# Kernel tuning notes

Hardware: AMD Instinct MI355X
Metric: run time of the kernel (lower is better)

## Reference

```python
import jax, jax.numpy as jnp
import numpy as np

CHANNELS = 256
TEMPERATURE = 0.1
VAR_LAMBDA = 0.001
N = 4096


def _pairwise_sq_dist(x, y):
    xx = jnp.sum(x * x, axis=-1)[:, None]
    yy = jnp.sum(y * y, axis=-1)[None, :]
    xy = jnp.einsum('ic,jc->ij', x, y)
    return xx + yy - 2.0 * xy


def _tcc_loss(emb_a, emb_b, idxes):
    scale = 1.0 / (CHANNELS * TEMPERATURE)
    sim_ab = -_pairwise_sq_dist(emb_a, emb_b) * scale            # [Na, Nb]
    softmaxed_sim_ab = jax.nn.softmax(sim_ab, axis=-1)
    soft_nn = softmaxed_sim_ab @ emb_b                            # [Na, C]
    sim_ba = -_pairwise_sq_dist(soft_nn, emb_a) * scale           # [Na, Na]
    beta = jax.nn.softmax(sim_ba, axis=-1)
    preds = jnp.sum(beta * idxes, axis=-1, keepdims=True)         # [Na, 1]
    pred_var = jnp.sum((idxes - preds) ** 2 * beta, axis=1)       # [Na]
    pred_var_log = jnp.log(pred_var)
    squared_error = (idxes - jnp.squeeze(preds, -1)) ** 2
    return jnp.sum(jnp.exp(-pred_var_log) * squared_error + VAR_LAMBDA * pred_var_log)


def setup_inputs() -> dict:
    key = jax.random.key(0)
    k1, k2 = jax.random.split(key)
    emb_a = jax.random.normal(k1, (1, N, CHANNELS), dtype=jnp.float32)
    emb_b = jax.random.normal(k2, (1, N, CHANNELS), dtype=jnp.float32)
    idx_a = jnp.arange(N, dtype=jnp.float32)
    idx_b = jnp.arange(N, dtype=jnp.float32)
    return {"emb_a": emb_a, "emb_b": emb_b, "idx_a": idx_a, "idx_b": idx_b}


def reference(emb_a, emb_b, idx_a, idx_b):
    a = jnp.squeeze(emb_a, 0)
    b = jnp.squeeze(emb_b, 0)
    loss_ab = _tcc_loss(a, b, idx_a)
    loss_ba = _tcc_loss(b, a, idx_b)
    return (loss_ab + loss_ba) / (a.shape[0] + b.shape[0])
```

## Files before the change

kernel.cpp:

```cpp
#include <hip/hip_runtime.h>

#define NTOT 4096
#define CH 256
#define SCALE 0.0390625f
#define LAM 0.001f

typedef unsigned short u16;
typedef __attribute__((ext_vector_type(8))) short short8;
typedef __attribute__((ext_vector_type(4))) float floatx4;

__device__ __forceinline__ float wave_sum64(float v) {
  #pragma unroll
  for (int o = 32; o; o >>= 1) v += __shfl_down(v, o, 64);
  return v;
}
__device__ __forceinline__ u16 f2bf(float f) {
  unsigned u = __float_as_uint(f);
  u += 0x7fffu + ((u >> 16) & 1u);
  return (u16)(u >> 16);
}
__device__ __forceinline__ float bf2f(u16 h) {
  return __uint_as_float(((unsigned)h) << 16);
}
__device__ __forceinline__ void gload_lds(const u16* g, void* l) {
  __builtin_amdgcn_global_load_lds((const __attribute__((address_space(1))) void*)g,
                                   (__attribute__((address_space(3))) void*)l, 16, 0, 0);
}
__device__ __forceinline__ void mm4x4(const short8 (&av)[4], const short8 (&bv)[4],
                                      floatx4 (&acc)[4][4]) {
  #pragma unroll
  for (int m = 0; m < 4; ++m)
    #pragma unroll
    for (int n = 0; n < 4; ++n)
      acc[m][n] = __builtin_amdgcn_mfma_f32_16x16x32_bf16(av[m], bv[n], acc[m][n], 0, 0, 0);
}

__global__ __launch_bounds__(64) void cvt_norm_k(const float* __restrict__ a,
                                                 const float* __restrict__ b,
                                                 u16* __restrict__ ab, u16* __restrict__ bb,
                                                 float* __restrict__ na, float* __restrict__ nb) {
  int row = blockIdx.x;
  const float* src; u16* dst; float* nd;
  if (row < NTOT) { src = a; dst = ab; nd = na; }
  else { row -= NTOT; src = b; dst = bb; nd = nb; }
  const float4 v = *reinterpret_cast<const float4*>(src + (size_t)row * CH + threadIdx.x * 4);
  const u16 h0 = f2bf(v.x), h1 = f2bf(v.y), h2 = f2bf(v.z), h3 = f2bf(v.w);
  uint2 st;
  st.x = (unsigned)h0 | ((unsigned)h1 << 16);
  st.y = (unsigned)h2 | ((unsigned)h3 << 16);
  *reinterpret_cast<uint2*>(dst + (size_t)row * CH + threadIdx.x * 4) = st;
  const float f0 = bf2f(h0), f1 = bf2f(h1), f2 = bf2f(h2), f3 = bf2f(h3);
  float s = f0 * f0 + f1 * f1 + f2 * f2 + f3 * f3;
  s = wave_sum64(s);
  if (threadIdx.x == 0) nd[row] = s;
}

__global__ __launch_bounds__(256) void transpose2_k(const u16* __restrict__ ab,
                                                    const u16* __restrict__ bb,
                                                    u16* __restrict__ at, u16* __restrict__ bt) {
  const u16* __restrict__ src = blockIdx.z ? bb : ab;
  u16* __restrict__ dst = blockIdx.z ? bt : at;
  __shared__ u16 t[32][33];
  const int bx = blockIdx.x * 32, by = blockIdx.y * 32;
  const int lx = threadIdx.x & 31, ly = threadIdx.x >> 5;
  #pragma unroll
  for (int i = 0; i < 32; i += 8)
    t[ly + i][lx] = src[(size_t)(by + ly + i) * CH + bx + lx];
  __syncthreads();
  #pragma unroll
  for (int i = 0; i < 32; i += 8)
    dst[(size_t)(bx + ly + i) * NTOT + by + lx] = t[lx][ly + i];
}

__global__ __launch_bounds__(256, 2) void gemm_exp_k(const u16* __restrict__ abf,
                                                     const u16* __restrict__ bbf,
                                                     const float* __restrict__ na,
                                                     const float* __restrict__ nb,
                                                     u16* __restrict__ E,
                                                     float* __restrict__ dnp) {
  const int wg = blockIdx.x;
  const int dir = wg >> 10;
  const int w = wg & 1023;
  const int xcd = w & 7;
  const int local = w >> 3;
  const int bx = local & 31;
  const int by = xcd * 4 + (local >> 5);

  const u16* __restrict__ A = dir ? bbf : abf;
  const u16* __restrict__ B = dir ? abf : bbf;
  const float* __restrict__ ny = dir ? na : nb;
  E += (size_t)dir * NTOT * NTOT;
  dnp += (size_t)dir * NTOT * 64;

  __shared__ u16 As[2][128][64];
  __shared__ u16 Bs[2][128][64];
  const int tid = threadIdx.x, wid = tid >> 6, lane = tid & 63;
  const int bn = bx * 128, bm = by * 128;
  const int wr = (wid >> 1) * 64, wc = (wid & 1) * 64;
  const int lr = lane & 15;

  auto stage = [&](int t, int bi) {
    const int k0 = t * 64;
    #pragma unroll
    for (int i = 0; i < 4; ++i) {
      const int lb = (wid + 4 * i) * 1024;
      const int db = lb + lane * 16;
      const int r = db >> 7;
      const int cb = (db & 127) ^ ((r & 7) << 4);
      gload_lds(A + (size_t)(bm + r) * CH + k0 + (cb >> 1), (char*)&As[bi][0][0] + lb);
      gload_lds(B + (size_t)(bn + r) * CH + k0 + (cb >> 1), (char*)&Bs[bi][0][0] + lb);
    }
  };

  floatx4 acc[4][4] = {};
  stage(0, 0);
  asm volatile("s_waitcnt vmcnt(0)" ::: "memory");
  __builtin_amdgcn_s_barrier();
  #pragma unroll
  for (int t = 0; t < 4; ++t) {
    if (t < 3) stage(t + 1, (t + 1) & 1);
    const int bi = t & 1;
    const char* Ab = (const char*)&As[bi][0][0];
    const char* Bb = (const char*)&Bs[bi][0][0];
    #pragma unroll
    for (int ks = 0; ks < 2; ++ks) {
      const int ob = ks * 64 + (lane >> 4) * 16;
      short8 af[4], bfr[4];
      #pragma unroll
      for (int m = 0; m < 4; ++m) {
        const int row = wr + m * 16 + lr;
        af[m] = *reinterpret_cast<const short8*>(Ab + row * 128 + (ob ^ ((row & 7) << 4)));
      }
      #pragma unroll
      for (int n = 0; n < 4; ++n) {
        const int row = wc + n * 16 + lr;
        bfr[n] = *reinterpret_cast<const short8*>(Bb + row * 128 + (ob ^ ((row & 7) << 4)));
      }
      mm4x4(af, bfr, acc);
    }
    if (t < 3) {
      asm volatile("s_waitcnt vmcnt(0)" ::: "memory");
      __builtin_amdgcn_s_barrier();
    }
  }
  float nyv[4];
  #pragma unroll
  for (int n = 0; n < 4; ++n) nyv[n] = ny[bn + wc + n * 16 + lr];
  float rowsum[4][4] = {};
  #pragma unroll
  for (int m = 0; m < 4; ++m) {
    const int rowb = bm + wr + m * 16 + (lane >> 4) * 4;
    #pragma unroll
    for (int n = 0; n < 4; ++n) {
      const int col = bn + wc + n * 16 + lr;
      #pragma unroll
      for (int r = 0; r < 4; ++r) {
        const float w = __expf((2.f * acc[m][n][r] - nyv[n]) * SCALE);
        E[(size_t)(rowb + r) * NTOT + col] = f2bf(w);
        rowsum[m][r] += w;
      }
    }
  }
  #pragma unroll
  for (int m = 0; m < 4; ++m) {
    const int rowb = bm + wr + m * 16 + (lane >> 4) * 4;
    #pragma unroll
    for (int r = 0; r < 4; ++r) {
      float s = rowsum[m][r];
      #pragma unroll
      for (int o = 1; o < 16; o <<= 1) s += __shfl_xor(s, o, 64);
      if (lr == 0) dnp[(size_t)(rowb + r) * 64 + bx * 2 + (wid & 1)] = s;
    }
  }
}

__global__ __launch_bounds__(256, 2) void gemm_qp_k(const u16* __restrict__ E,
                                                    const u16* __restrict__ att,
                                                    const u16* __restrict__ btt,
                                                    float* __restrict__ Qp) {
  const int wg = blockIdx.x;
  const int dk = wg & 7;
  const int j = wg >> 3;
  const int dir = dk >> 2, kz = dk & 3;
  const int bxi = j & 1, byi = j >> 1;

  const u16* __restrict__ A = E + (size_t)dir * NTOT * NTOT;
  const u16* __restrict__ B = dir ? att : btt;
  float* __restrict__ C = Qp + (size_t)dir * 4 * NTOT * CH + (size_t)kz * NTOT * CH;
  const int k0base = kz * (NTOT / 4);

  __shared__ u16 As[2][128][64];
  __shared__ u16 Bs[2][128][64];
  const int tid = threadIdx.x, wid = tid >> 6, lane = tid & 63;
  const int bn = bxi * 128, bm = byi * 128;
  const int wr = (wid >> 1) * 64, wc = (wid & 1) * 64;
  const int lr = lane & 15;

  auto stage = [&](int t, int bi) {
    const int k0 = k0base + t * 64;
    #pragma unroll
    for (int i = 0; i < 4; ++i) {
      const int lb = (wid + 4 * i) * 1024;
      const int db = lb + lane * 16;
      const int r = db >> 7;
      const int cb = (db & 127) ^ ((r & 7) << 4);
      gload_lds(A + (size_t)(bm + r) * NTOT + k0 + (cb >> 1), (char*)&As[bi][0][0] + lb);
      gload_lds(B + (size_t)(bn + r) * NTOT + k0 + (cb >> 1), (char*)&Bs[bi][0][0] + lb);
    }
  };

  floatx4 acc[4][4] = {};
  stage(0, 0);
  asm volatile("s_waitcnt vmcnt(0)" ::: "memory");
  __builtin_amdgcn_s_barrier();
  for (int t = 0; t < 16; ++t) {
    if (t < 15) stage(t + 1, (t + 1) & 1);
    const int bi = t & 1;
    const char* Ab = (const char*)&As[bi][0][0];
    const char* Bb = (const char*)&Bs[bi][0][0];
    #pragma unroll
    for (int ks = 0; ks < 2; ++ks) {
      const int ob = ks * 64 + (lane >> 4) * 16;
      short8 af[4], bfr[4];
      #pragma unroll
      for (int m = 0; m < 4; ++m) {
        const int row = wr + m * 16 + lr;
        af[m] = *reinterpret_cast<const short8*>(Ab + row * 128 + (ob ^ ((row & 7) << 4)));
      }
      #pragma unroll
      for (int n = 0; n < 4; ++n) {
        const int row = wc + n * 16 + lr;
        bfr[n] = *reinterpret_cast<const short8*>(Bb + row * 128 + (ob ^ ((row & 7) << 4)));
      }
      mm4x4(af, bfr, acc);
    }
    asm volatile("s_waitcnt vmcnt(0)" ::: "memory");
    __builtin_amdgcn_s_barrier();
  }
  #pragma unroll
  for (int m = 0; m < 4; ++m) {
    const int row = bm + wr + m * 16 + (lane >> 4) * 4;
    #pragma unroll
    for (int n = 0; n < 4; ++n) {
      const int col = bn + wc + n * 16 + lr;
      #pragma unroll
      for (int r = 0; r < 4; ++r)
        C[(size_t)(row + r) * CH + col] = acc[m][n][r];
    }
  }
}

__global__ __launch_bounds__(256) void reduce_q_k(const float* __restrict__ Qp,
                                                  const float* __restrict__ dnp,
                                                  u16* __restrict__ Qb) {
  const int dir = blockIdx.z;
  Qp += (size_t)dir * 4 * NTOT * CH;
  dnp += (size_t)dir * NTOT * 64;
  Qb += (size_t)dir * NTOT * CH;
  const int row = blockIdx.x, tid = threadIdx.x;
  __shared__ float sdn;
  if (tid < 64) {
    float s = dnp[(size_t)row * 64 + tid];
    s = wave_sum64(s);
    if (tid == 0) sdn = 1.0f / s;
  }
  __syncthreads();
  const float rdn = sdn;
  const size_t o = (size_t)row * CH + tid;
  const size_t st = (size_t)NTOT * CH;
  const float q = (Qp[o] + Qp[o + st] + Qp[o + 2 * st] + Qp[o + 3 * st]) * rdn;
  Qb[o] = f2bf(q);
}

__global__ __launch_bounds__(256, 2) void flash_stats_k(const u16* __restrict__ Qball,
                                                        const u16* __restrict__ abf,
                                                        const u16* __restrict__ bbf,
                                                        const float* __restrict__ na,
                                                        const float* __restrict__ nb,
                                                        const float* __restrict__ idxa,
                                                        const float* __restrict__ idxb,
                                                        float4* __restrict__ statsp) {
  const int wg = blockIdx.x;
  const int dir = wg >> 9;
  const int w = wg & 511;
  const int xcd = w & 7;
  const int local = w >> 3;
  const int bx = local & 15;
  const int by = xcd * 4 + (local >> 4);

  const u16* __restrict__ Qb = Qball + (size_t)dir * NTOT * CH;
  const u16* __restrict__ X = dir ? bbf : abf;
  const float* __restrict__ nx = dir ? nb : na;
  const float* __restrict__ idx = dir ? idxb : idxa;
  statsp += (size_t)dir * NTOT * 32;

  __shared__ u16 As[2][128][64];
  __shared__ u16 Bs[2][128][64];
  const int tid = threadIdx.x, wid = tid >> 6, lane = tid & 63;
  const int bm = by * 128;
  const int jbase = bx * 256;
  const int wr = (wid >> 1) * 64, wc = (wid & 1) * 64;
  const int lr = lane & 15;

  auto stage = [&](int t, int bi) {
    const int k0 = (t & 3) * 64;
    const int bn = jbase + (t >> 2) * 128;
    #pragma unroll
    for (int i = 0; i < 4; ++i) {
      const int lb = (wid + 4 * i) * 1024;
      const int db = lb + lane * 16;
      const int r = db >> 7;
      const int cb = (db & 127) ^ ((r & 7) << 4);
      gload_lds(Qb + (size_t)(bm + r) * CH + k0 + (cb >> 1), (char*)&As[bi][0][0] + lb);
      gload_lds(X + (size_t)(bn + r) * CH + k0 + (cb >> 1), (char*)&Bs[bi][0][0] + lb);
    }
  };

  float cen[4][4];
  #pragma unroll
  for (int m = 0; m < 4; ++m) {
    const int rowb = bm + wr + m * 16 + (lane >> 4) * 4;
    #pragma unroll
    for (int r = 0; r < 4; ++r) cen[m][r] = idx[rowb + r];
  }
  float s0[4][4] = {}, s1[4][4] = {}, s2[4][4] = {};
  floatx4 acc[4][4] = {};

  stage(0, 0);
  asm volatile("s_waitcnt vmcnt(0)" ::: "memory");
  __builtin_amdgcn_s_barrier();
  #pragma unroll
  for (int t = 0; t < 8; ++t) {
    if (t < 7) stage(t + 1, (t + 1) & 1);
    const int bi = t & 1;
    const char* Ab = (const char*)&As[bi][0][0];
    const char* Bb = (const char*)&Bs[bi][0][0];
    #pragma unroll
    for (int ks = 0; ks < 2; ++ks) {
      const int ob = ks * 64 + (lane >> 4) * 16;
      short8 af[4], bfr[4];
      #pragma unroll
      for (int m = 0; m < 4; ++m) {
        const int row = wr + m * 16 + lr;
        af[m] = *reinterpret_cast<const short8*>(Ab + row * 128 + (ob ^ ((row & 7) << 4)));
      }
      #pragma unroll
      for (int n = 0; n < 4; ++n) {
        const int row = wc + n * 16 + lr;
        bfr[n] = *reinterpret_cast<const short8*>(Bb + row * 128 + (ob ^ ((row & 7) << 4)));
      }
      mm4x4(af, bfr, acc);
    }
    if ((t & 3) == 3) {
      const int bn = jbase + (t >> 2) * 128;
      #pragma unroll
      for (int n = 0; n < 4; ++n) {
        const int col = bn + wc + n * 16 + lr;
        const float nxv = nx[col];
        const float iv = idx[col];
        #pragma unroll
        for (int m = 0; m < 4; ++m) {
          #pragma unroll
          for (int r = 0; r < 4; ++r) {
            const float w = __expf((2.f * acc[m][n][r] - nxv) * SCALE);
            const float d = iv - cen[m][r];
            s0[m][r] += w;
            s1[m][r] += w * d;
            s2[m][r] += w * d * d;
            acc[m][n][r] = 0.f;
          }
        }
      }
    }
    if (t < 7) {
      asm volatile("s_waitcnt vmcnt(0)" ::: "memory");
      __builtin_amdgcn_s_barrier();
    }
  }
  #pragma unroll
  for (int m = 0; m < 4; ++m) {
    const int rowb = bm + wr + m * 16 + (lane >> 4) * 4;
    #pragma unroll
    for (int r = 0; r < 4; ++r) {
      float a = s0[m][r], b = s1[m][r], c = s2[m][r];
      #pragma unroll
      for (int o = 1; o < 16; o <<= 1) {
        a += __shfl_xor(a, o, 64);
        b += __shfl_xor(b, o, 64);
        c += __shfl_xor(c, o, 64);
      }
      if (lr == 0)
        statsp[(size_t)(rowb + r) * 32 + bx * 2 + (wid & 1)] = make_float4(a, b, c, 0.f);
    }
  }
}

__global__ __launch_bounds__(256) void stats_combine_k(const float4* __restrict__ statsp,
                                                       float* __restrict__ terms) {
  const int row = blockIdx.x * 256 + threadIdx.x;
  float S0 = 0.f, S1 = 0.f, S2 = 0.f;
  #pragma unroll
  for (int p = 0; p < 32; ++p) {
    const float4 v = statsp[(size_t)row * 32 + p];
    S0 += v.x; S1 += v.y; S2 += v.z;
  }
  const float mu = S1 / S0;
  const float var = S2 / S0 - mu * mu;
  terms[row] = mu * mu / var + LAM * logf(var);
}

__global__ __launch_bounds__(256) void final_reduce_k(const float* __restrict__ terms,
                                                      float* __restrict__ out) {
  float s = 0.f;
  for (int i = threadIdx.x; i < 2 * NTOT; i += 256) s += terms[i];
  __shared__ float red[4];
  s = wave_sum64(s);
  if ((threadIdx.x & 63) == 0) red[threadIdx.x >> 6] = s;
  __syncthreads();
  if (threadIdx.x == 0) out[0] = (red[0] + red[1] + red[2] + red[3]) * (1.0f / (2.0f * NTOT));
}

extern "C" void kernel_launch(void* const* d_in, const int* in_sizes, int n_in,
                              void* d_out, int out_size, void* d_ws, size_t ws_size,
                              hipStream_t stream) {
  const float* a    = (const float*)d_in[0];
  const float* b    = (const float*)d_in[1];
  const float* idxa = (const float*)d_in[2];
  const float* idxb = (const float*)d_in[3];
  float* out = (float*)d_out;
  char* ws = (char*)d_ws;

  size_t off = 0;
  u16*    E    = (u16*)(ws + off);    off += 2 * (size_t)NTOT * NTOT * 2;
  float*  Qp   = (float*)(ws + off);  off += 2 * 4 * (size_t)NTOT * CH * 4;
  u16*    Qb   = (u16*)(ws + off);    off += 2 * (size_t)NTOT * CH * 2;
  u16*    abf  = (u16*)(ws + off);    off += (size_t)NTOT * CH * 2;
  u16*    bbf  = (u16*)(ws + off);    off += (size_t)NTOT * CH * 2;
  u16*    att  = (u16*)(ws + off);    off += (size_t)NTOT * CH * 2;
  u16*    btt  = (u16*)(ws + off);    off += (size_t)NTOT * CH * 2;
  float*  na   = (float*)(ws + off);  off += (size_t)NTOT * 4;
  float*  nb   = (float*)(ws + off);  off += (size_t)NTOT * 4;
  float*  dnp  = (float*)(ws + off);  off += 2 * (size_t)NTOT * 64 * 4;
  float4* stp  = (float4*)(ws + off); off += 2 * (size_t)NTOT * 32 * 16;
  float*  terms = (float*)(ws + off);

  cvt_norm_k<<<2 * NTOT, 64, 0, stream>>>(a, b, abf, bbf, na, nb);
  transpose2_k<<<dim3(CH / 32, NTOT / 32, 2), 256, 0, stream>>>(abf, bbf, att, btt);
  gemm_exp_k<<<2048, 256, 0, stream>>>(abf, bbf, na, nb, E, dnp);
  gemm_qp_k<<<512, 256, 0, stream>>>(E, att, btt, Qp);
  reduce_q_k<<<dim3(NTOT, 1, 2), 256, 0, stream>>>(Qp, dnp, Qb);
  flash_stats_k<<<1024, 256, 0, stream>>>(Qb, abf, bbf, na, nb, idxa, idxb, stp);
  stats_combine_k<<<2 * NTOT / 256, 256, 0, stream>>>(stp, terms);
  final_reduce_k<<<1, 256, 0, stream>>>(terms, out);
}
```

Baseline: 135.9 us.

## Compute both direction exp tiles from one shared A·Bᵀ GEMM

The two similarity directions share the same dot-product matrix, since B·Aᵀ is the transpose of A·Bᵀ. The kernel now runs one 32x32 grid of GEMM tiles instead of two. Each tile writes the ab exponentials directly and builds the ba exponentials through an LDS transpose before writing them out coalesced. Column sums become the partial denominators for the ba direction. This halves the MFMA work and operand loads. In exchange it adds a second exp per element, LDS transpose traffic, and drops the previous XCD-aware block mapping.

```diff
diff --git a/kernel.cpp b/kernel.cpp
--- a/kernel.cpp
+++ b/kernel.cpp
@@ -34,6 +34,7 @@
     for (int n = 0; n < 4; ++n)
       acc[m][n] = __builtin_amdgcn_mfma_f32_16x16x32_bf16(av[m], bv[n], acc[m][n], 0, 0, 0);
 }
+__device__ __forceinline__ int swz128(int row) { return (row & 7) << 4; }
 
 __global__ __launch_bounds__(64) void cvt_norm_k(const float* __restrict__ a,
                                                  const float* __restrict__ b,
@@ -78,26 +79,17 @@
                                                      const float* __restrict__ nb,
                                                      u16* __restrict__ E,
                                                      float* __restrict__ dnp) {
-  const int wg = blockIdx.x;
-  const int dir = wg >> 10;
-  const int w = wg & 1023;
-  const int xcd = w & 7;
-  const int local = w >> 3;
-  const int bx = local & 31;
-  const int by = xcd * 4 + (local >> 5);
-
-  const u16* __restrict__ A = dir ? bbf : abf;
-  const u16* __restrict__ B = dir ? abf : bbf;
-  const float* __restrict__ ny = dir ? na : nb;
-  E += (size_t)dir * NTOT * NTOT;
-  dnp += (size_t)dir * NTOT * 64;
-
-  __shared__ u16 As[2][128][64];
-  __shared__ u16 Bs[2][128][64];
+  const int bx = blockIdx.x, by = blockIdx.y;
+  const int bn = bx * 128, bm = by * 128;
+  u16* __restrict__ Eab = E;
+  u16* __restrict__ Eba = E + (size_t)NTOT * NTOT;
+  float* __restrict__ dnp0 = dnp;
+  float* __restrict__ dnp1 = dnp + (size_t)NTOT * 64;
+
+  __shared__ u16 smem[32768];
   const int tid = threadIdx.x, wid = tid >> 6, lane = tid & 63;
-  const int bn = bx * 128, bm = by * 128;
   const int wr = (wid >> 1) * 64, wc = (wid & 1) * 64;
-  const int lr = lane & 15;
+  const int lr = lane & 15, g = lane >> 4;
 
   auto stage = [&](int t, int bi) {
     const int k0 = t * 64;
@@ -106,9 +98,9 @@
       const int lb = (wid + 4 * i) * 1024;
       const int db = lb + lane * 16;
       const int r = db >> 7;
-      const int cb = (db & 127) ^ ((r & 7) << 4);
-      gload_lds(A + (size_t)(bm + r) * CH + k0 + (cb >> 1), (char*)&As[bi][0][0] + lb);
-      gload_lds(B + (size_t)(bn + r) * CH + k0 + (cb >> 1), (char*)&Bs[bi][0][0] + lb);
+      const int cb = (db & 127) ^ swz128(r);
+      gload_lds(abf + (size_t)(bm + r) * CH + k0 + (cb >> 1), (char*)smem + bi * 16384 + lb);
+      gload_lds(bbf + (size_t)(bn + r) * CH + k0 + (cb >> 1), (char*)smem + 32768 + bi * 16384 + lb);
     }
   };
 
@@ -120,21 +112,21 @@
   for (int t = 0; t < 4; ++t) {
     if (t < 3) stage(t + 1, (t + 1) & 1);
     const int bi = t & 1;
-    const char* Ab = (const char*)&As[bi][0][0];
-    const char* Bb = (const char*)&Bs[bi][0][0];
+    const char* Ab = (const char*)smem + bi * 16384;
+    const char* Bb = (const char*)smem + 32768 + bi * 16384;
     #pragma unroll
     for (int ks = 0; ks < 2; ++ks) {
-      const int ob = ks * 64 + (lane >> 4) * 16;
+      const int ob = ks * 64 + g * 16;
       short8 af[4], bfr[4];
       #pragma unroll
       for (int m = 0; m < 4; ++m) {
         const int row = wr + m * 16 + lr;
-        af[m] = *reinterpret_cast<const short8*>(Ab + row * 128 + (ob ^ ((row & 7) << 4)));
+        af[m] = *reinterpret_cast<const short8*>(Ab + row * 128 + (ob ^ swz128(row)));
       }
       #pragma unroll
       for (int n = 0; n < 4; ++n) {
         const int row = wc + n * 16 + lr;
-        bfr[n] = *reinterpret_cast<const short8*>(Bb + row * 128 + (ob ^ ((row & 7) << 4)));
+        bfr[n] = *reinterpret_cast<const short8*>(Bb + row * 128 + (ob ^ swz128(row)));
       }
       mm4x4(af, bfr, acc);
     }
@@ -143,34 +135,66 @@
       __builtin_amdgcn_s_barrier();
     }
   }
-  float nyv[4];
-  #pragma unroll
-  for (int n = 0; n < 4; ++n) nyv[n] = ny[bn + wc + n * 16 + lr];
-  float rowsum[4][4] = {};
-  #pragma unroll
-  for (int m = 0; m < 4; ++m) {
-    const int rowb = bm + wr + m * 16 + (lane >> 4) * 4;
+  __syncthreads();
+  u16 (*Lba)[136] = reinterpret_cast<u16 (*)[136]>(smem);
+
+  float nbv[4], nav[4][4];
+  #pragma unroll
+  for (int n = 0; n < 4; ++n) nbv[n] = nb[bn + wc + n * 16 + lr];
+  #pragma unroll
+  for (int m = 0; m < 4; ++m) {
+    const int rowb = bm + wr + m * 16 + g * 4;
+    #pragma unroll
+    for (int r = 0; r < 4; ++r) nav[m][r] = na[rowb + r];
+  }
+
+  float rowsum[4][4] = {}, colsum[4] = {};
+  #pragma unroll
+  for (int m = 0; m < 4; ++m) {
+    const int rowb = bm + wr + m * 16 + g * 4;
+    const int ilb = wr + m * 16 + g * 4;
     #pragma unroll
     for (int n = 0; n < 4; ++n) {
       const int col = bn + wc + n * 16 + lr;
+      const int jl = wc + n * 16 + lr;
       #pragma unroll
       for (int r = 0; r < 4; ++r) {
-        const float w = __expf((2.f * acc[m][n][r] - nyv[n]) * SCALE);
-        E[(size_t)(rowb + r) * NTOT + col] = f2bf(w);
-        rowsum[m][r] += w;
-      }
-    }
-  }
-  #pragma unroll
-  for (int m = 0; m < 4; ++m) {
-    const int rowb = bm + wr + m * 16 + (lane >> 4) * 4;
+        const float s2 = 2.f * acc[m][n][r];
+        const float w0 = __expf((s2 - nbv[n]) * SCALE);
+        Eab[(size_t)(rowb + r) * NTOT + col] = f2bf(w0);
+        rowsum[m][r] += w0;
+        const float w1 = __expf((s2 - nav[m][r]) * SCALE);
+        colsum[n] += w1;
+        Lba[jl][ilb + r] = f2bf(w1);
+      }
+    }
+  }
+  #pragma unroll
+  for (int m = 0; m < 4; ++m) {
+    const int rowb = bm + wr + m * 16 + g * 4;
     #pragma unroll
     for (int r = 0; r < 4; ++r) {
       float s = rowsum[m][r];
       #pragma unroll
       for (int o = 1; o < 16; o <<= 1) s += __shfl_xor(s, o, 64);
-      if (lr == 0) dnp[(size_t)(rowb + r) * 64 + bx * 2 + (wid & 1)] = s;
-    }
+      if (lr == 0) dnp0[(size_t)(rowb + r) * 64 + bx * 2 + (wid & 1)] = s;
+    }
+  }
+  #pragma unroll
+  for (int n = 0; n < 4; ++n) {
+    float v = colsum[n];
+    v += __shfl_xor(v, 16, 64);
+    v += __shfl_xor(v, 32, 64);
+    if (g == 0)
+      dnp1[(size_t)(bn + wc + n * 16 + lr) * 64 + by * 2 + (wid >> 1)] = v;
+  }
+  __syncthreads();
+  #pragma unroll
+  for (int p = 0; p < 8; ++p) {
+    const int jl = (tid >> 4) + p * 16;
+    const int il = (tid & 15) * 8;
+    const short8 v = *reinterpret_cast<const short8*>(&Lba[jl][il]);
+    *reinterpret_cast<short8*>(&Eba[(size_t)(bn + jl) * NTOT + bm + il]) = v;
   }
 }
 
@@ -203,7 +227,7 @@
       const int lb = (wid + 4 * i) * 1024;
       const int db = lb + lane * 16;
       const int r = db >> 7;
-      const int cb = (db & 127) ^ ((r & 7) << 4);
+      const int cb = (db & 127) ^ swz128(r);
       gload_lds(A + (size_t)(bm + r) * NTOT + k0 + (cb >> 1), (char*)&As[bi][0][0] + lb);
       gload_lds(B + (size_t)(bn + r) * NTOT + k0 + (cb >> 1), (char*)&Bs[bi][0][0] + lb);
     }
@@ -225,12 +249,12 @@
       #pragma unroll
       for (int m = 0; m < 4; ++m) {
         const int row = wr + m * 16 + lr;
-        af[m] = *reinterpret_cast<const short8*>(Ab + row * 128 + (ob ^ ((row & 7) << 4)));
+        af[m] = *reinterpret_cast<const short8*>(Ab + row * 128 + (ob ^ swz128(row)));
       }
       #pragma unroll
       for (int n = 0; n < 4; ++n) {
         const int row = wc + n * 16 + lr;
-        bfr[n] = *reinterpret_cast<const short8*>(Bb + row * 128 + (ob ^ ((row & 7) << 4)));
+        bfr[n] = *reinterpret_cast<const short8*>(Bb + row * 128 + (ob ^ swz128(row)));
       }
       mm4x4(af, bfr, acc);
     }
@@ -310,7 +334,7 @@
       const int lb = (wid + 4 * i) * 1024;
       const int db = lb + lane * 16;
       const int r = db >> 7;
-      const int cb = (db & 127) ^ ((r & 7) << 4);
+      const int cb = (db & 127) ^ swz128(r);
       gload_lds(Qb + (size_t)(bm + r) * CH + k0 + (cb >> 1), (char*)&As[bi][0][0] + lb);
       gload_lds(X + (size_t)(bn + r) * CH + k0 + (cb >> 1), (char*)&Bs[bi][0][0] + lb);
     }
@@ -342,12 +366,12 @@
       #pragma unroll
       for (int m = 0; m < 4; ++m) {
         const int row = wr + m * 16 + lr;
-        af[m] = *reinterpret_cast<const short8*>(Ab + row * 128 + (ob ^ ((row & 7) << 4)));
+        af[m] = *reinterpret_cast<const short8*>(Ab + row * 128 + (ob ^ swz128(row)));
       }
       #pragma unroll
       for (int n = 0; n < 4; ++n) {
         const int row = wc + n * 16 + lr;
-        bfr[n] = *reinterpret_cast<const short8*>(Bb + row * 128 + (ob ^ ((row & 7) << 4)));
+        bfr[n] = *reinterpret_cast<const short8*>(Bb + row * 128 + (ob ^ swz128(row)));
       }
       mm4x4(af, bfr, acc);
     }
@@ -362,11 +386,11 @@
         for (int m = 0; m < 4; ++m) {
           #pragma unroll
           for (int r = 0; r < 4; ++r) {
-            const float w = __expf((2.f * acc[m][n][r] - nxv) * SCALE);
+            const float w2 = __expf((2.f * acc[m][n][r] - nxv) * SCALE);
             const float d = iv - cen[m][r];
-            s0[m][r] += w;
-            s1[m][r] += w * d;
-            s2[m][r] += w * d * d;
+            s0[m][r] += w2;
+            s1[m][r] += w2 * d;
+            s2[m][r] += w2 * d * d;
             acc[m][n][r] = 0.f;
           }
         }
@@ -446,7 +470,7 @@
 
   cvt_norm_k<<<2 * NTOT, 64, 0, stream>>>(a, b, abf, bbf, na, nb);
   transpose2_k<<<dim3(CH / 32, NTOT / 32, 2), 256, 0, stream>>>(abf, bbf, att, btt);
-  gemm_exp_k<<<2048, 256, 0, stream>>>(abf, bbf, na, nb, E, dnp);
+  gemm_exp_k<<<dim3(32, 32), 256, 0, stream>>>(abf, bbf, na, nb, E, dnp);
   gemm_qp_k<<<512, 256, 0, stream>>>(E, att, btt, Qp);
   reduce_q_k<<<dim3(NTOT, 1, 2), 256, 0, stream>>>(Qp, dnp, Qb);
   flash_stats_k<<<1024, 256, 0, stream>>>(Qb, abf, bbf, na, nb, idxa, idxb, stp);
```

Result: faster. 125.0 us (-8.0%).
